# Kernel tuning notes

Hardware: AMD Instinct MI355X
Metric: run time of the kernel (lower is better)

The kernel has to match this reference:

```python
import jax, jax.numpy as jnp
import numpy as np

N, E, IN_DIM, OUT_DIM, NTYPE, QDIM = 32, 512, 300, 300, 4, 300
SLOPE = 0.2  # lrelu:0.2


def setup_inputs() -> dict:
    key = jax.random.key(0)
    ks = jax.random.split(key, 8)
    return {
        "input_state": jax.random.normal(ks[0], (N, E, IN_DIM), jnp.float32),
        "adj": jax.random.randint(ks[1], (N, E, E), 0, NTYPE + 1, dtype=jnp.int32),
        "node_mask": jax.random.uniform(ks[2], (N, E, 1), jnp.float32),
        "query_vec": jax.random.normal(ks[3], (N, QDIM), jnp.float32),
        "W_type": jax.random.normal(ks[4], (NTYPE, IN_DIM, OUT_DIM), jnp.float32) * 0.02,
        "a_type": jax.random.normal(ks[5], (NTYPE, 2 * OUT_DIM), jnp.float32) * 0.02,
        "qattn_W1": jax.random.normal(ks[6], (NTYPE, QDIM, 2 * OUT_DIM), jnp.float32) * 0.02,
        "qattn_W2": jax.random.normal(ks[7], (NTYPE, 2 * OUT_DIM, 2 * OUT_DIM), jnp.float32) * 0.02,
    }


def reference(input_state, adj, node_mask, query_vec, W_type, a_type, qattn_W1, qattn_W2):
    # Faithful GAT head. The original builds an [N,E,E,2d] concat tensor; since
    # a_input[n,i,j] = [h_i, h_j] and the gate broadcasts over (i,j), the score
    # decomposes exactly as lrelu((h*g1)@a1 [:,i,None] + (h*g2)@a2 [:,None,j]).
    lrelu = lambda x: jnp.where(x >= 0, x, SLOPE * x)
    scores = jnp.zeros(adj.shape, jnp.float32)
    h = None
    for i in range(NTYPE):
        h = jnp.einsum("ned,df->nef", input_state, W_type[i])  # [N,E,d] (dropout: eval no-op)
        q_gate = jax.nn.relu(query_vec @ qattn_W1[i])
        q_gate = jax.nn.sigmoid(q_gate @ qattn_W2[i])          # [N,2d]
        g1, g2 = q_gate[:, :OUT_DIM], q_gate[:, OUT_DIM:]
        a1, a2 = a_type[i][:OUT_DIM], a_type[i][OUT_DIM:]
        s_src = jnp.einsum("ned,d->ne", h * g1[:, None, :], a1)  # contributes along i
        s_dst = jnp.einsum("ned,d->ne", h * g2[:, None, :], a2)  # contributes along j
        score = lrelu(s_src[:, :, None] + s_dst[:, None, :])      # [N,E,E]
        scores = scores + jnp.where(adj == i + 1, score, 0.0)
    scores = jnp.where(adj > 0, scores, jnp.float32(-1e30))
    h = h * node_mask  # note: original applies mask to h from the LAST edge type
    coefs = jax.nn.softmax(scores, axis=2)
    return jnp.einsum("nij,njd->nid", coefs, h)
```

## Files before the change

### kernel.cpp

```cpp
#include <hip/hip_runtime.h>
#include <hip/hip_bf16.h>

#define Nn   32
#define Ee   512
#define DIN  300
#define DOUT 300
#define NT   4
#define QD   300
#define SLOPE 0.2f
#define ROWS 64
#define CPAD 320
#define SSTR 516
#define USTR 65

typedef __attribute__((ext_vector_type(8))) short bf16x8;
typedef __attribute__((ext_vector_type(4))) float f32x4;
typedef __attribute__((ext_vector_type(4))) unsigned short u16x4;

__device__ inline unsigned short f2bf(float x) {
    __hip_bfloat16 h = __float2bfloat16(x);
    return *reinterpret_cast<unsigned short*>(&h);
}
__device__ inline float bf2f(unsigned short u) {
    __hip_bfloat16 h = *reinterpret_cast<__hip_bfloat16*>(&u);
    return __bfloat162float(h);
}

__global__ __launch_bounds__(256) void prep_kernel(
    const float* __restrict__ W3,
    unsigned short* __restrict__ W3T_hi,
    unsigned short* __restrict__ W3T_lo,
    unsigned short* __restrict__ UTh,
    unsigned short* __restrict__ UTl,
    unsigned short* __restrict__ GTh,
    unsigned short* __restrict__ GTl)
{
    int idx = blockIdx.x * 256 + threadIdx.x;
    if (idx < 320 * 320) {
        int c = idx / 320, k = idx - c * 320;
        float v = (c < DOUT && k < DIN) ? W3[(size_t)k * DOUT + c] : 0.f;
        unsigned short h = f2bf(v);
        W3T_hi[idx] = h;
        W3T_lo[idx] = f2bf(v - bf2f(h));
    }
    if (idx < 32 * 16 * 320) { UTh[idx] = 0; UTl[idx] = 0; }
    if (idx < 4 * 64 * 320)  { GTh[idx] = 0; GTl[idx] = 0; }
}

__global__ __launch_bounds__(256) void gates1_part_kernel(
    const float* __restrict__ q,
    const float* __restrict__ W1,
    float* __restrict__ t1p)
{
    int i = blockIdx.y, z = blockIdx.z;
    int idx = blockIdx.x * 256 + threadIdx.x;
    int n = idx / 600, j = idx - n * 600;
    const float* W1i = W1 + (size_t)i * QD * 600;
    const float* qn = q + n * QD;
    int k0 = z * 75;
    float a0 = 0.f;
    #pragma unroll 5
    for (int k = k0; k < k0 + 75; ++k)
        a0 += qn[k] * W1i[(size_t)k * 600 + j];
    t1p[((size_t)(z * NT + i) * Nn + n) * 600 + j] = a0;
}

__global__ __launch_bounds__(256) void gates1_fin_kernel(
    const float* __restrict__ t1p, float* __restrict__ t1)
{
    int i = blockIdx.y;
    int idx = blockIdx.x * 256 + threadIdx.x;
    size_t o = ((size_t)i * Nn) * 600 + idx;
    float s = t1p[o] + t1p[o + 76800] + t1p[o + 2 * 76800] + t1p[o + 3 * 76800];
    t1[o] = fmaxf(s, 0.f);
}

__global__ __launch_bounds__(256) void gates2_part_kernel(
    const float* __restrict__ t1,
    const float* __restrict__ W2,
    float* __restrict__ gp)
{
    int i = blockIdx.y, z = blockIdx.z;
    int idx = blockIdx.x * 256 + threadIdx.x;
    int n = idx / 600, j = idx - n * 600;
    const float* W2i = W2 + (size_t)i * 600 * 600;
    const float* tn = t1 + ((size_t)i * Nn + n) * 600;
    int k0 = z * 150;
    float a0 = 0.f, a1 = 0.f;
    #pragma unroll 5
    for (int k = k0; k < k0 + 150; k += 2) {
        a0 += tn[k]     * W2i[(size_t)k * 600 + j];
        a1 += tn[k + 1] * W2i[(size_t)(k + 1) * 600 + j];
    }
    gp[((size_t)(z * NT + i) * Nn + n) * 600 + j] = a0 + a1;
}

__global__ __launch_bounds__(256) void gates2_fin_kernel(
    const float* __restrict__ gp,
    const float* __restrict__ a,
    unsigned short* __restrict__ GTh,
    unsigned short* __restrict__ GTl)
{
    int i = blockIdx.y;
    int idx = blockIdx.x * 256 + threadIdx.x;
    int n = idx / 600, j = idx - n * 600;
    size_t o = ((size_t)i * Nn + n) * 600 + j;
    float s = gp[o] + gp[o + 76800] + gp[o + 2 * 76800] + gp[o + 3 * 76800];
    float w = (1.f / (1.f + __expf(-s))) * a[(size_t)i * 600 + j];
    int s2 = (j >= DOUT) ? 1 : 0;
    int d = j - s2 * DOUT;
    int c = 2 * n + s2;
    size_t go = ((size_t)i * 64 + c) * 320 + d;
    unsigned short h = f2bf(w);
    GTh[go] = h;
    GTl[go] = f2bf(w - bf2f(h));
}

__global__ __launch_bounds__(256) void uvec_mfma_kernel(
    const float* __restrict__ W,
    const unsigned short* __restrict__ GTh,
    const unsigned short* __restrict__ GTl,
    unsigned short* __restrict__ UTh,
    unsigned short* __restrict__ UTl)
{
    int mc = blockIdx.x, i = blockIdx.y;
    int tid = threadIdx.x, wv = tid >> 6, lane = tid & 63;
    int g = lane >> 4, cr = lane & 15;
    int m0 = mc * 64 + wv * 16;
    int arow = m0 + cr;
    const float* wr = W + (size_t)i * DIN * DOUT
                        + (size_t)(arow < DIN ? arow : 0) * DOUT;

    f32x4 acc[4];
    #pragma unroll
    for (int nt = 0; nt < 4; ++nt) acc[nt] = (f32x4){0.f, 0.f, 0.f, 0.f};

    for (int ks = 0; ks < 10; ++ks) {
        int k0 = ks * 32 + 8 * g;
        float x8[8];
        if (ks < 9) {
            f32x4 v0 = *(const f32x4*)(wr + k0);
            f32x4 v1 = *(const f32x4*)(wr + k0 + 4);
            #pragma unroll
            for (int j = 0; j < 4; ++j) { x8[j] = v0[j]; x8[4 + j] = v1[j]; }
        } else {
            #pragma unroll
            for (int j = 0; j < 8; ++j) {
                int d = k0 + j;
                x8[j] = (d < DOUT) ? wr[d] : 0.f;
            }
        }
        bf16x8 ahi, alo;
        #pragma unroll
        for (int j = 0; j < 8; ++j) {
            unsigned short h = f2bf(x8[j]);
            ahi[j] = (short)h;
            alo[j] = (short)f2bf(x8[j] - bf2f(h));
        }
        #pragma unroll
        for (int nt = 0; nt < 4; ++nt) {
            size_t bo = ((size_t)i * 64 + nt * 16 + cr) * 320 + k0;
            bf16x8 bh = *(const bf16x8*)(GTh + bo);
            bf16x8 bl = *(const bf16x8*)(GTl + bo);
            acc[nt] = __builtin_amdgcn_mfma_f32_16x16x32_bf16(ahi, bh, acc[nt], 0, 0, 0);
            acc[nt] = __builtin_amdgcn_mfma_f32_16x16x32_bf16(ahi, bl, acc[nt], 0, 0, 0);
            acc[nt] = __builtin_amdgcn_mfma_f32_16x16x32_bf16(alo, bh, acc[nt], 0, 0, 0);
        }
    }

    int krow = m0 + 4 * g;
    if (krow < DIN) {
        #pragma unroll
        for (int nt = 0; nt < 4; ++nt) {
            int c = nt * 16 + cr;
            int n = c >> 1, s = c & 1;
            size_t base = ((size_t)n * 16 + 2 * i + s) * 320 + krow;
            u16x4 h4, l4;
            #pragma unroll
            for (int q = 0; q < 4; ++q) {
                float v = acc[nt][q];
                unsigned short h = f2bf(v);
                h4[q] = h;
                l4[q] = f2bf(v - bf2f(h));
            }
            *(u16x4*)(UTh + base) = h4;
            *(u16x4*)(UTl + base) = l4;
        }
    }
}

__global__ __launch_bounds__(256) void hm_mfma_kernel(
    const float* __restrict__ X,
    const float* __restrict__ mask,
    const unsigned short* __restrict__ W3T_hi,
    const unsigned short* __restrict__ W3T_lo,
    const unsigned short* __restrict__ UTh,
    const unsigned short* __restrict__ UTl,
    unsigned short* __restrict__ hmT_hi,
    unsigned short* __restrict__ hmT_lo,
    float* __restrict__ ssrc,
    float* __restrict__ sdst)
{
    int tid = threadIdx.x, wv = tid >> 6, lane = tid & 63;
    int g = lane >> 4, cr = lane & 15;
    size_t row0 = (size_t)blockIdx.x * 32;
    int n = (int)(row0 >> 9), j0 = (int)(row0 & 511);

    __shared__ float maskL[32];
    if (tid < 32) maskL[tid] = mask[row0 + tid];
    __syncthreads();

    f32x4 acc[5][2];
    f32x4 sacc[2];
    #pragma unroll
    for (int a = 0; a < 5; ++a)
        #pragma unroll
        for (int m = 0; m < 2; ++m) acc[a][m] = (f32x4){0.f, 0.f, 0.f, 0.f};
    sacc[0] = (f32x4){0.f, 0.f, 0.f, 0.f};
    sacc[1] = (f32x4){0.f, 0.f, 0.f, 0.f};

    const float* xr0 = X + (row0 + cr) * DIN;
    const float* xr1 = X + (row0 + 16 + cr) * DIN;

    for (int ks = 0; ks < 10; ++ks) {
        int k0 = ks * 32 + 8 * g;
        bf16x8 ahi[2], alo[2];
        #pragma unroll
        for (int m = 0; m < 2; ++m) {
            const float* xr = m ? xr1 : xr0;
            float x8[8];
            if (ks < 9) {
                f32x4 v0 = *(const f32x4*)(xr + k0);
                f32x4 v1 = *(const f32x4*)(xr + k0 + 4);
                #pragma unroll
                for (int j = 0; j < 4; ++j) { x8[j] = v0[j]; x8[4 + j] = v1[j]; }
            } else {
                #pragma unroll
                for (int j = 0; j < 8; ++j) {
                    int k = k0 + j;
                    x8[j] = (k < DIN) ? xr[k] : 0.f;
                }
            }
            #pragma unroll
            for (int j = 0; j < 8; ++j) {
                unsigned short h = f2bf(x8[j]);
                ahi[m][j] = (short)h;
                alo[m][j] = (short)f2bf(x8[j] - bf2f(h));
            }
        }
        #pragma unroll
        for (int ntl = 0; ntl < 5; ++ntl) {
            int c = (wv + 4 * ntl) * 16 + cr;
            bf16x8 bh = *(const bf16x8*)(W3T_hi + (size_t)c * 320 + k0);
            bf16x8 bl = *(const bf16x8*)(W3T_lo + (size_t)c * 320 + k0);
            #pragma unroll
            for (int m = 0; m < 2; ++m) {
                acc[ntl][m] = __builtin_amdgcn_mfma_f32_16x16x32_bf16(ahi[m], bh, acc[ntl][m], 0, 0, 0);
                acc[ntl][m] = __builtin_amdgcn_mfma_f32_16x16x32_bf16(ahi[m], bl, acc[ntl][m], 0, 0, 0);
                acc[ntl][m] = __builtin_amdgcn_mfma_f32_16x16x32_bf16(alo[m], bh, acc[ntl][m], 0, 0, 0);
            }
        }
        if (wv == 0) {
            bf16x8 uh = *(const bf16x8*)(UTh + ((size_t)n * 16 + cr) * 320 + k0);
            bf16x8 ul = *(const bf16x8*)(UTl + ((size_t)n * 16 + cr) * 320 + k0);
            #pragma unroll
            for (int m = 0; m < 2; ++m) {
                sacc[m] = __builtin_amdgcn_mfma_f32_16x16x32_bf16(ahi[m], uh, sacc[m], 0, 0, 0);
                sacc[m] = __builtin_amdgcn_mfma_f32_16x16x32_bf16(ahi[m], ul, sacc[m], 0, 0, 0);
                sacc[m] = __builtin_amdgcn_mfma_f32_16x16x32_bf16(alo[m], uh, sacc[m], 0, 0, 0);
            }
        }
    }

    #pragma unroll
    for (int ntl = 0; ntl < 5; ++ntl) {
        int c = (wv + 4 * ntl) * 16 + cr;
        #pragma unroll
        for (int m = 0; m < 2; ++m) {
            u16x4 h4, l4;
            #pragma unroll
            for (int qq = 0; qq < 4; ++qq) {
                float v = acc[ntl][m][qq] * maskL[m * 16 + 4 * g + qq];
                unsigned short h = f2bf(v);
                h4[qq] = h;
                l4[qq] = f2bf(v - bf2f(h));
            }
            size_t off = ((size_t)(n * CPAD + c)) * Ee + j0 + m * 16 + 4 * g;
            *(u16x4*)(hmT_hi + off) = h4;
            *(u16x4*)(hmT_lo + off) = l4;
        }
    }

    if (wv == 0 && cr < 8) {
        int i = cr >> 1;
        float* dst = (cr & 1) ? sdst : ssrc;
        #pragma unroll
        for (int m = 0; m < 2; ++m)
            #pragma unroll
            for (int qq = 0; qq < 4; ++qq)
                dst[((size_t)i * Nn + n) * Ee + j0 + m * 16 + 4 * g + qq] = sacc[m][qq];
    }
}

__global__ __launch_bounds__(512, 1) void attn64_kernel(
    const int*   __restrict__ adj,
    const float* __restrict__ ssrc,
    const float* __restrict__ sdst,
    const unsigned short* __restrict__ hmT_hi,
    const unsigned short* __restrict__ hmT_lo,
    float* __restrict__ out)
{
    int f  = blockIdx.x;
    int n  = (f & 7) * 4 + ((f >> 3) & 3);
    int rt = f >> 5;
    int tid = threadIdx.x;
    int row0 = rt * ROWS;

    __shared__ unsigned uni[Ee * USTR];
    __shared__ float sdl[NT * Ee];
    __shared__ float ssl[NT * 65];
    float* S = (float*)uni;

    for (int idx = tid; idx < NT * Ee; idx += 512) {
        int i = idx >> 9, j = idx & (Ee - 1);
        sdl[idx] = sdst[((size_t)i * Nn + n) * Ee + j];
    }
    if (tid < NT * ROWS) {
        int i = tid >> 6, r = tid & 63;
        ssl[i * 65 + r] = ssrc[((size_t)i * Nn + n) * Ee + row0 + r];
    }
    __syncthreads();

    const int* adjb = adj + ((size_t)n * Ee + row0) * Ee;
    for (int idx4 = tid; idx4 < (ROWS * Ee) / 4; idx4 += 512) {
        int r  = idx4 >> 7;
        int jb = (idx4 & 127) << 2;
        int4 t4 = *(const int4*)(adjb + (idx4 << 2));
        int tv[4] = {t4.x, t4.y, t4.z, t4.w};
        f32x4 v4;
        #pragma unroll
        for (int u = 0; u < 4; ++u) {
            int t = tv[u];
            int j = jb + u;
            float v;
            if (t > 0) {
                float x = ssl[(t - 1) * 65 + r] + sdl[(t - 1) * Ee + j];
                v = (x >= 0.f) ? x : SLOPE * x;
            } else {
                v = -1e30f;
            }
            v4[u] = v;
        }
        *(f32x4*)(S + r * SSTR + jb) = v4;
    }
    __syncthreads();

    int wv = tid >> 6, lane = tid & 63;
    float vals[8][8];
    float inv[8];
    #pragma unroll
    for (int rr = 0; rr < 8; ++rr) {
        int r = wv * 8 + rr;
        float m = -3.0e38f;
        #pragma unroll
        for (int k = 0; k < 8; ++k) {
            vals[rr][k] = S[r * SSTR + lane + 64 * k];
            m = fmaxf(m, vals[rr][k]);
        }
        #pragma unroll
        for (int off = 32; off; off >>= 1) m = fmaxf(m, __shfl_xor(m, off));
        float s = 0.f;
        #pragma unroll
        for (int k = 0; k < 8; ++k) {
            vals[rr][k] = __expf(vals[rr][k] - m);
            s += vals[rr][k];
        }
        #pragma unroll
        for (int off = 32; off; off >>= 1) s += __shfl_xor(s, off);
        inv[rr] = 1.f / s;
    }
    __syncthreads();

    #pragma unroll
    for (int rr = 0; rr < 8; ++rr) {
        int r = wv * 8 + rr;
        #pragma unroll
        for (int k = 0; k < 8; ++k) {
            float v = vals[rr][k] * inv[rr];
            unsigned short hi = f2bf(v);
            unsigned short lo = f2bf(v - bf2f(hi));
            uni[(lane + 64 * k) * USTR + r] = ((unsigned)hi << 16) | (unsigned)lo;
        }
    }
    __syncthreads();

    int g = lane >> 4, cr = lane & 15;
    f32x4 acc[3][4];
    #pragma unroll
    for (int t = 0; t < 3; ++t)
        #pragma unroll
        for (int m = 0; m < 4; ++m) acc[t][m] = (f32x4){0.f, 0.f, 0.f, 0.f};

#define LOADB(BH, BL, KS) do {                                              \
    int kk_ = (KS) * 32 + 8 * g;                                            \
    _Pragma("unroll")                                                       \
    for (int t_ = 0; t_ < 3; ++t_) {                                        \
        int ct_ = wv + 8 * t_;                                              \
        if (ct_ < 20) {                                                     \
            size_t off_ = ((size_t)(n * CPAD + ct_ * 16 + cr)) * Ee + kk_;  \
            BH[t_] = *(const bf16x8*)(hmT_hi + off_);                       \
            BL[t_] = *(const bf16x8*)(hmT_lo + off_);                       \
        }                                                                   \
    }                                                                       \
} while (0)

#define PVSTEP(KS, BH, BL) do {                                             \
    int kk_ = (KS) * 32;                                                    \
    bf16x8 ahi_[4], alo_[4];                                                \
    _Pragma("unroll")                                                       \
    for (int m_ = 0; m_ < 4; ++m_) {                                        \
        _Pragma("unroll")                                                   \
        for (int j_ = 0; j_ < 8; ++j_) {                                    \
            unsigned v_ = uni[(kk_ + 8 * g + j_) * USTR + m_ * 16 + cr];    \
            ahi_[m_][j_] = (short)(v_ >> 16);                               \
            alo_[m_][j_] = (short)(v_ & 0xffffu);                           \
        }                                                                   \
    }                                                                       \
    __builtin_amdgcn_s_setprio(1);                                          \
    _Pragma("unroll")                                                       \
    for (int t_ = 0; t_ < 3; ++t_) {                                        \
        if (wv + 8 * t_ < 20) {                                             \
            _Pragma("unroll")                                               \
            for (int m_ = 0; m_ < 4; ++m_) {                                \
                acc[t_][m_] = __builtin_amdgcn_mfma_f32_16x16x32_bf16(ahi_[m_], BH[t_], acc[t_][m_], 0, 0, 0); \
                acc[t_][m_] = __builtin_amdgcn_mfma_f32_16x16x32_bf16(ahi_[m_], BL[t_], acc[t_][m_], 0, 0, 0); \
                acc[t_][m_] = __builtin_amdgcn_mfma_f32_16x16x32_bf16(alo_[m_], BH[t_], acc[t_][m_], 0, 0, 0); \
            }                                                               \
        }                                                                   \
    }                                                                       \
    __builtin_amdgcn_s_setprio(0);                                          \
} while (0)

    bf16x8 bhA[3], blA[3], bhB[3], blB[3];
    LOADB(bhA, blA, 0);
    #pragma unroll
    for (int ks = 0; ks < 16; ks += 2) {
        LOADB(bhB, blB, ks + 1);
        PVSTEP(ks, bhA, blA);
        if (ks + 2 < 16) LOADB(bhA, blA, ks + 2);
        PVSTEP(ks + 1, bhB, blB);
    }
#undef LOADB
#undef PVSTEP

    #pragma unroll
    for (int t = 0; t < 3; ++t) {
        int ct = wv + 8 * t;
        if (ct < 20) {
            int c = ct * 16 + cr;
            if (c < DOUT) {
                #pragma unroll
                for (int m = 0; m < 4; ++m) {
                    #pragma unroll
                    for (int q = 0; q < 4; ++q) {
                        int erow = row0 + m * 16 + 4 * g + q;
                        out[((size_t)n * Ee + erow) * DOUT + c] = acc[t][m][q];
                    }
                }
            }
        }
    }
}

extern "C" void kernel_launch(void* const* d_in, const int* in_sizes, int n_in,
                              void* d_out, int out_size, void* d_ws, size_t ws_size,
                              hipStream_t stream) {
    const float* input_state = (const float*)d_in[0];
    const int*   adj         = (const int*)  d_in[1];
    const float* node_mask   = (const float*)d_in[2];
    const float* query_vec   = (const float*)d_in[3];
    const float* W_type      = (const float*)d_in[4];
    const float* a_type      = (const float*)d_in[5];
    const float* qattn_W1    = (const float*)d_in[6];
    const float* qattn_W2    = (const float*)d_in[7];
    float* out = (float*)d_out;

    float* ws   = (float*)d_ws;
    float* t1   = ws;
    float* ssrc = t1   + 76800;
    float* sdst = ssrc + 65536;
    unsigned short* W3T_hi = (unsigned short*)(sdst + 65536);
    unsigned short* W3T_lo = W3T_hi + 320 * 320;
    unsigned short* GTh    = W3T_lo + 320 * 320;
    unsigned short* GTl    = GTh + 4 * 64 * 320;
    unsigned short* UTh    = GTl + 4 * 64 * 320;
    unsigned short* UTl    = UTh + 32 * 16 * 320;
    unsigned short* hmT_hi = UTl + 32 * 16 * 320;
    unsigned short* hmT_lo = hmT_hi + (size_t)Nn * CPAD * Ee;
    float* t1p = (float*)(hmT_lo + (size_t)Nn * CPAD * Ee);
    float* gp  = t1p + 307200;

    hipLaunchKernelGGL(prep_kernel, dim3(640), dim3(256), 0, stream,
                       W_type + 3 * DIN * DOUT, W3T_hi, W3T_lo, UTh, UTl, GTh, GTl);
    hipLaunchKernelGGL(gates1_part_kernel, dim3(75, NT, 4), dim3(256), 0, stream,
                       query_vec, qattn_W1, t1p);
    hipLaunchKernelGGL(gates1_fin_kernel, dim3(75, NT), dim3(256), 0, stream,
                       t1p, t1);
    hipLaunchKernelGGL(gates2_part_kernel, dim3(75, NT, 4), dim3(256), 0, stream,
                       t1, qattn_W2, gp);
    hipLaunchKernelGGL(gates2_fin_kernel, dim3(75, NT), dim3(256), 0, stream,
                       gp, a_type, GTh, GTl);
    hipLaunchKernelGGL(uvec_mfma_kernel, dim3(5, NT), dim3(256), 0, stream,
                       W_type, GTh, GTl, UTh, UTl);
    hipLaunchKernelGGL(hm_mfma_kernel, dim3((Nn * Ee) / 32), dim3(256), 0, stream,
                       input_state, node_mask, W3T_hi, W3T_lo, UTh, UTl,
                       hmT_hi, hmT_lo, ssrc, sdst);
    hipLaunchKernelGGL(attn64_kernel, dim3(256), dim3(512), 0, stream,
                       adj, ssrc, sdst, hmT_hi, hmT_lo, out);
}
```

Measured before the change: 129.9 us.

## Enlarge hm_mfma row tile to 64 rows with 8 waves; swizzle sdst LDS

The hm_mfma kernel now handles 64 rows per block with 512 threads. Eight waves split the 20 column tiles, so each W3T fragment load feeds four row tiles instead of two, and weight traffic per row is halved. Each wave does its own f32-to-bf16 split of the X rows, so that conversion work is duplicated across more waves, and waves 4-7 get only two column tiles while waves 0-3 get three, leaving the split uneven. Separately, the per-type sdst vector in the attention kernel's LDS is stored XOR-swizzled to reduce bank conflicts on the gathered score reads.

```diff
diff --git a/kernel.cpp b/kernel.cpp
--- a/kernel.cpp
+++ b/kernel.cpp
@@ -25,6 +25,7 @@
     __hip_bfloat16 h = *reinterpret_cast<__hip_bfloat16*>(&u);
     return __bfloat162float(h);
 }
+__device__ inline int swzj(int j) { return j ^ ((j >> 5) & 3); }
 
 __global__ __launch_bounds__(256) void prep_kernel(
     const float* __restrict__ W3,
@@ -189,7 +190,7 @@
     }
 }
 
-__global__ __launch_bounds__(256) void hm_mfma_kernel(
+__global__ __launch_bounds__(512) void hm_mfma_kernel(
     const float* __restrict__ X,
     const float* __restrict__ mask,
     const unsigned short* __restrict__ W3T_hi,
@@ -203,31 +204,34 @@
 {
     int tid = threadIdx.x, wv = tid >> 6, lane = tid & 63;
     int g = lane >> 4, cr = lane & 15;
-    size_t row0 = (size_t)blockIdx.x * 32;
+    size_t row0 = (size_t)blockIdx.x * 64;
     int n = (int)(row0 >> 9), j0 = (int)(row0 & 511);
 
-    __shared__ float maskL[32];
-    if (tid < 32) maskL[tid] = mask[row0 + tid];
+    __shared__ float maskL[64];
+    if (tid < 64) maskL[tid] = mask[row0 + tid];
     __syncthreads();
 
-    f32x4 acc[5][2];
-    f32x4 sacc[2];
-    #pragma unroll
-    for (int a = 0; a < 5; ++a)
-        #pragma unroll
-        for (int m = 0; m < 2; ++m) acc[a][m] = (f32x4){0.f, 0.f, 0.f, 0.f};
-    sacc[0] = (f32x4){0.f, 0.f, 0.f, 0.f};
-    sacc[1] = (f32x4){0.f, 0.f, 0.f, 0.f};
-
-    const float* xr0 = X + (row0 + cr) * DIN;
+    f32x4 acc[3][4];
+    f32x4 sacc[4];
+    #pragma unroll
+    for (int t = 0; t < 3; ++t)
+        #pragma unroll
+        for (int m = 0; m < 4; ++m) acc[t][m] = (f32x4){0.f, 0.f, 0.f, 0.f};
+    #pragma unroll
+    for (int m = 0; m < 4; ++m) sacc[m] = (f32x4){0.f, 0.f, 0.f, 0.f};
+
+    const float* xr0 = X + (row0 +      cr) * DIN;
     const float* xr1 = X + (row0 + 16 + cr) * DIN;
+    const float* xr2 = X + (row0 + 32 + cr) * DIN;
+    const float* xr3 = X + (row0 + 48 + cr) * DIN;
+    const float* xrs[4] = {xr0, xr1, xr2, xr3};
 
     for (int ks = 0; ks < 10; ++ks) {
         int k0 = ks * 32 + 8 * g;
-        bf16x8 ahi[2], alo[2];
-        #pragma unroll
-        for (int m = 0; m < 2; ++m) {
-            const float* xr = m ? xr1 : xr0;
+        bf16x8 ahi[4], alo[4];
+        #pragma unroll
+        for (int m = 0; m < 4; ++m) {
+            const float* xr = xrs[m];
             float x8[8];
             if (ks < 9) {
                 f32x4 v0 = *(const f32x4*)(xr + k0);
@@ -249,22 +253,25 @@
             }
         }
         #pragma unroll
-        for (int ntl = 0; ntl < 5; ++ntl) {
-            int c = (wv + 4 * ntl) * 16 + cr;
-            bf16x8 bh = *(const bf16x8*)(W3T_hi + (size_t)c * 320 + k0);
-            bf16x8 bl = *(const bf16x8*)(W3T_lo + (size_t)c * 320 + k0);
-            #pragma unroll
-            for (int m = 0; m < 2; ++m) {
-                acc[ntl][m] = __builtin_amdgcn_mfma_f32_16x16x32_bf16(ahi[m], bh, acc[ntl][m], 0, 0, 0);
-                acc[ntl][m] = __builtin_amdgcn_mfma_f32_16x16x32_bf16(ahi[m], bl, acc[ntl][m], 0, 0, 0);
-                acc[ntl][m] = __builtin_amdgcn_mfma_f32_16x16x32_bf16(alo[m], bh, acc[ntl][m], 0, 0, 0);
+        for (int t = 0; t < 3; ++t) {
+            int ct = wv + 8 * t;
+            if (ct < 20) {
+                int c = ct * 16 + cr;
+                bf16x8 bh = *(const bf16x8*)(W3T_hi + (size_t)c * 320 + k0);
+                bf16x8 bl = *(const bf16x8*)(W3T_lo + (size_t)c * 320 + k0);
+                #pragma unroll
+                for (int m = 0; m < 4; ++m) {
+                    acc[t][m] = __builtin_amdgcn_mfma_f32_16x16x32_bf16(ahi[m], bh, acc[t][m], 0, 0, 0);
+                    acc[t][m] = __builtin_amdgcn_mfma_f32_16x16x32_bf16(ahi[m], bl, acc[t][m], 0, 0, 0);
+                    acc[t][m] = __builtin_amdgcn_mfma_f32_16x16x32_bf16(alo[m], bh, acc[t][m], 0, 0, 0);
+                }
             }
         }
         if (wv == 0) {
             bf16x8 uh = *(const bf16x8*)(UTh + ((size_t)n * 16 + cr) * 320 + k0);
             bf16x8 ul = *(const bf16x8*)(UTl + ((size_t)n * 16 + cr) * 320 + k0);
             #pragma unroll
-            for (int m = 0; m < 2; ++m) {
+            for (int m = 0; m < 4; ++m) {
                 sacc[m] = __builtin_amdgcn_mfma_f32_16x16x32_bf16(ahi[m], uh, sacc[m], 0, 0, 0);
                 sacc[m] = __builtin_amdgcn_mfma_f32_16x16x32_bf16(ahi[m], ul, sacc[m], 0, 0, 0);
                 sacc[m] = __builtin_amdgcn_mfma_f32_16x16x32_bf16(alo[m], uh, sacc[m], 0, 0, 0);
@@ -273,21 +280,24 @@
     }
 
     #pragma unroll
-    for (int ntl = 0; ntl < 5; ++ntl) {
-        int c = (wv + 4 * ntl) * 16 + cr;
-        #pragma unroll
-        for (int m = 0; m < 2; ++m) {
-            u16x4 h4, l4;
-            #pragma unroll
-            for (int qq = 0; qq < 4; ++qq) {
-                float v = acc[ntl][m][qq] * maskL[m * 16 + 4 * g + qq];
-                unsigned short h = f2bf(v);
-                h4[qq] = h;
-                l4[qq] = f2bf(v - bf2f(h));
-            }
-            size_t off = ((size_t)(n * CPAD + c)) * Ee + j0 + m * 16 + 4 * g;
-            *(u16x4*)(hmT_hi + off) = h4;
-            *(u16x4*)(hmT_lo + off) = l4;
+    for (int t = 0; t < 3; ++t) {
+        int ct = wv + 8 * t;
+        if (ct < 20) {
+            int c = ct * 16 + cr;
+            #pragma unroll
+            for (int m = 0; m < 4; ++m) {
+                u16x4 h4, l4;
+                #pragma unroll
+                for (int qq = 0; qq < 4; ++qq) {
+                    float v = acc[t][m][qq] * maskL[m * 16 + 4 * g + qq];
+                    unsigned short h = f2bf(v);
+                    h4[qq] = h;
+                    l4[qq] = f2bf(v - bf2f(h));
+                }
+                size_t off = ((size_t)(n * CPAD + c)) * Ee + j0 + m * 16 + 4 * g;
+                *(u16x4*)(hmT_hi + off) = h4;
+                *(u16x4*)(hmT_lo + off) = l4;
+            }
         }
     }
 
@@ -295,7 +305,7 @@
         int i = cr >> 1;
         float* dst = (cr & 1) ? sdst : ssrc;
         #pragma unroll
-        for (int m = 0; m < 2; ++m)
+        for (int m = 0; m < 4; ++m)
             #pragma unroll
             for (int qq = 0; qq < 4; ++qq)
                 dst[((size_t)i * Nn + n) * Ee + j0 + m * 16 + 4 * g + qq] = sacc[m][qq];
@@ -323,7 +333,7 @@
 
     for (int idx = tid; idx < NT * Ee; idx += 512) {
         int i = idx >> 9, j = idx & (Ee - 1);
-        sdl[idx] = sdst[((size_t)i * Nn + n) * Ee + j];
+        sdl[i * Ee + swzj(j)] = sdst[((size_t)i * Nn + n) * Ee + j];
     }
     if (tid < NT * ROWS) {
         int i = tid >> 6, r = tid & 63;
@@ -335,16 +345,16 @@
     for (int idx4 = tid; idx4 < (ROWS * Ee) / 4; idx4 += 512) {
         int r  = idx4 >> 7;
         int jb = (idx4 & 127) << 2;
+        int xw = (jb >> 5) & 3;
         int4 t4 = *(const int4*)(adjb + (idx4 << 2));
         int tv[4] = {t4.x, t4.y, t4.z, t4.w};
         f32x4 v4;
         #pragma unroll
         for (int u = 0; u < 4; ++u) {
             int t = tv[u];
-            int j = jb + u;
             float v;
             if (t > 0) {
-                float x = ssl[(t - 1) * 65 + r] + sdl[(t - 1) * Ee + j];
+                float x = ssl[(t - 1) * 65 + r] + sdl[(t - 1) * Ee + jb + (u ^ xw)];
                 v = (x >= 0.f) ? x : SLOPE * x;
             } else {
                 v = -1e30f;
@@ -512,7 +522,7 @@
                        gp, a_type, GTh, GTl);
     hipLaunchKernelGGL(uvec_mfma_kernel, dim3(5, NT), dim3(256), 0, stream,
                        W_type, GTh, GTl, UTh, UTl);
-    hipLaunchKernelGGL(hm_mfma_kernel, dim3((Nn * Ee) / 32), dim3(256), 0, stream,
+    hipLaunchKernelGGL(hm_mfma_kernel, dim3((Nn * Ee) / 64), dim3(512), 0, stream,
                        input_state, node_mask, W3T_hi, W3T_lo, UTh, UTl,
                        hmT_hi, hmT_lo, ssrc, sdst);
     hipLaunchKernelGGL(attn64_kernel, dim3(256), dim3(512), 0, stream,
```

Measured after the change: 121.3 us. 1.07x faster.
